# Performance work log

Measured on AMD Instinct MI355X. Metric: run time of the kernel, lower is better.

The kernel has to match this reference:

```python
import jax, jax.numpy as jnp
import numpy as np

B, S, D = 8, 1024, 1024      # batch, seq_len, inp_dim
H, HD = 8, 64                # head_num, head_dim
HID = H * HD                 # hidden_dim = 512
P = 2 * D                    # p_factor * inp_dim = 2048
K = 4                        # causal conv kernel size
EPS = 1e-6
CAP = 15.0                   # soft cap for i/f gates


def _layernorm(x, g, b):
    mu = jnp.mean(x, -1, keepdims=True)
    var = jnp.var(x, -1, keepdims=True)
    return (x - mu) * jax.lax.rsqrt(var + EPS) * g + b


def _soft_cap(v):
    return CAP * jnp.tanh(v / CAP)


def _causal_conv_feat(x, w, b):
    # Conv1d(1,1,K) applied over the FEATURE axis of each timestep (as in the
    # torch code: x_t.unsqueeze(1) -> (bs,1,P)), causal left pad of K-1.
    L = x.shape[-1]
    xp = jnp.pad(x, ((0, 0), (0, 0), (K - 1, 0)))
    out = b
    for m in range(K):
        out = out + w[m] * xp[..., m:m + L]
    return out


def _forward(x, ln_g, ln_b, mh_g, mh_b, W_up_l, b_up_l, W_up_r, b_up_r,
             W_down, b_down, conv_w, conv_b, W_skip, b_skip, W_i, b_i,
             W_f, b_f, W_o, b_o, W_q, b_q, W_k, b_k, W_v, b_v):
    Bs, Sl, _ = x.shape
    xn = _layernorm(x, ln_g, ln_b)
    x_t = xn @ W_up_l.T + b_up_l                      # (B,S,P)
    r_t = xn @ W_up_r.T + b_up_r                      # (B,S,HID)
    x_c = jax.nn.silu(_causal_conv_feat(x_t, conv_w, conv_b))
    x_skip = x_c @ W_skip.T + b_skip                  # (B,S,HID)
    q = (x_c @ W_q.T + b_q).reshape(Bs, Sl, H, HD)
    k = (x_c @ W_k.T + b_k).reshape(Bs, Sl, H, HD) / float(np.sqrt(HD))
    v = (x_t @ W_v.T + b_v).reshape(Bs, Sl, H, HD)
    i_pre = _soft_cap(x_c @ W_i.T + b_i)              # (B,S,H)
    f_pre = _soft_cap(x_c @ W_f.T + b_f)              # (B,S,H)
    o = jax.nn.sigmoid(x_t @ W_o.T + b_o)             # (B,S,HID)

    def step(carry, inp):
        c, n, m = carry
        qt, kt, vt, it, ft = inp
        m_t = jnp.maximum(ft + m, it)
        ie = jnp.exp(it - m_t)
        fe = jnp.exp(ft - m_t + m)
        c = fe[:, :, None, None] * c + ie[:, :, None, None] * jnp.einsum('bhd,bhe->bhde', vt, kt)
        n = fe[:, :, None] * n + ie[:, :, None] * kt
        num = jnp.einsum('bhde,bhe->bhd', c, qt)
        den = jnp.maximum(jnp.sum(n * qt, -1, keepdims=True), 1.0)
        return (c, n, m_t), num / den

    c0 = jnp.zeros((Bs, H, HD, HD), x.dtype)
    n0 = jnp.ones((Bs, H, HD), x.dtype)
    m0 = jnp.zeros((Bs, H), x.dtype)
    seq = tuple(jnp.moveaxis(a, 1, 0) for a in (q, k, v, i_pre, f_pre))
    _, hs = jax.lax.scan(step, (c0, n0, m0), seq)     # hs: (S,B,H,HD)
    h = o * jnp.moveaxis(hs, 0, 1).reshape(Bs, Sl, HID)
    hn = _layernorm(h.reshape(Bs, Sl, H, HD), mh_g, mh_b).reshape(Bs, Sl, HID)
    out = (hn + x_skip) * jax.nn.silu(r_t)
    return out @ W_down.T + b_down + x


def setup_inputs() -> dict:
    key = jax.random.key(0)
    ks = jax.random.split(key, 16)

    def w(kk, shape):
        return jax.random.normal(kk, shape, jnp.float32) / np.sqrt(shape[-1]).astype(np.float32)

    return {
        'x': jax.random.normal(ks[0], (B, S, D), jnp.float32),
        'ln_g': jnp.ones((D,), jnp.float32), 'ln_b': jnp.zeros((D,), jnp.float32),
        'mh_g': jnp.ones((H, HD), jnp.float32), 'mh_b': jnp.zeros((H, HD), jnp.float32),
        'W_up_l': w(ks[1], (P, D)), 'b_up_l': jnp.zeros((P,), jnp.float32),
        'W_up_r': w(ks[2], (HID, D)), 'b_up_r': jnp.zeros((HID,), jnp.float32),
        'W_down': w(ks[3], (D, HID)), 'b_down': jnp.zeros((D,), jnp.float32),
        'conv_w': jax.random.normal(ks[4], (K,), jnp.float32) * 0.3,
        'conv_b': jnp.zeros((), jnp.float32),
        'W_skip': w(ks[5], (HID, P)), 'b_skip': jnp.zeros((HID,), jnp.float32),
        'W_i': w(ks[6], (H, P)), 'b_i': jnp.zeros((H,), jnp.float32),
        'W_f': w(ks[7], (H, P)), 'b_f': jnp.zeros((H,), jnp.float32),
        'W_o': w(ks[8], (HID, P)), 'b_o': jnp.zeros((HID,), jnp.float32),
        'W_q': w(ks[9], (HID, P)), 'b_q': jnp.zeros((HID,), jnp.float32),
        'W_k': w(ks[10], (HID, P)), 'b_k': jnp.zeros((HID,), jnp.float32),
        'W_v': w(ks[11], (HID, P)), 'b_v': jnp.zeros((HID,), jnp.float32),
    }


def reference(x, ln_g, ln_b, mh_g, mh_b, W_up_l, b_up_l, W_up_r, b_up_r,
              W_down, b_down, conv_w, conv_b, W_skip, b_skip, W_i, b_i,
              W_f, b_f, W_o, b_o, W_q, b_q, W_k, b_k, W_v, b_v):
    return _forward(x, ln_g, ln_b, mh_g, mh_b, W_up_l, b_up_l, W_up_r, b_up_r,
                    W_down, b_down, conv_w, conv_b, W_skip, b_skip, W_i, b_i,
                    W_f, b_f, W_o, b_o, W_q, b_q, W_k, b_k, W_v, b_v)
```

## Files before the change

kernel.cpp:

```cpp
#include <hip/hip_runtime.h>
#include <hip/hip_bf16.h>
#include <math.h>

#define Bq 8
#define Sq 1024
#define Dq 1024
#define Hq 8
#define HDq 64
#define HIDq 512
#define Pq 2048
#define EPSq 1e-6f
#define CAPq 15.0f
#define NCq 16
#define CLq 64
#define ARENA_SH 4096
#define BUF_SH   (4 * ARENA_SH)
#define GEMM_SMEM_BYTES (2 * BUF_SH * 2)

typedef __attribute__((ext_vector_type(8))) short short8;
typedef __attribute__((ext_vector_type(4))) float f32x4v;
typedef __hip_bfloat16 bf16;

__device__ inline void split2(float v, bf16& h, bf16& l) {
  h = __float2bfloat16(v);
  l = __float2bfloat16(v - __bfloat162float(h));
}

__device__ inline float bfs2f(short s) {
  bf16 t = *(const bf16*)&s;
  return __bfloat162float(t);
}

__global__ __launch_bounds__(256) void cvtw_all(
    const float* __restrict__ s0, const float* __restrict__ s1,
    const float* __restrict__ s2, const float* __restrict__ s3,
    const float* __restrict__ s4, const float* __restrict__ s5,
    const float* __restrict__ s6, const float* __restrict__ s7,
    bf16* __restrict__ hi, bf16* __restrict__ lo)
{
  int u = blockIdx.x * 256 + threadIdx.x;
  const float* src; int segBase;
  if      (u <  524288) { src = s0; segBase = 0;       }
  else if (u <  655360) { src = s1; segBase = 524288;  }
  else if (u <  917504) { src = s2; segBase = 655360;  }
  else if (u < 1179648) { src = s3; segBase = 917504;  }
  else if (u < 1441792) { src = s4; segBase = 1179648; }
  else if (u < 1703936) { src = s5; segBase = 1441792; }
  else if (u < 1966080) { src = s6; segBase = 1703936; }
  else                  { src = s7; segBase = 1966080; }
  float4 v = ((const float4*)src)[u - segBase];
  size_t o = (size_t)u * 4;
  bf16 h, l;
  split2(v.x, h, l); hi[o+0] = h; lo[o+0] = l;
  split2(v.y, h, l); hi[o+1] = h; lo[o+1] = l;
  split2(v.z, h, l); hi[o+2] = h; lo[o+2] = l;
  split2(v.w, h, l); hi[o+3] = h; lo[o+3] = l;
}

__global__ __launch_bounds__(256) void ln_kernel(const float* __restrict__ x,
    const float* __restrict__ g, const float* __restrict__ b,
    bf16* __restrict__ yh, bf16* __restrict__ yl)
{
  int row = blockIdx.x;
  int tid = threadIdx.x;
  const float* xr = x + (size_t)row * Dq;
  float v[4]; float s = 0.f, s2 = 0.f;
  #pragma unroll
  for (int i = 0; i < 4; i++) { v[i] = xr[tid + 256*i]; s += v[i]; s2 += v[i]*v[i]; }
  #pragma unroll
  for (int mm = 32; mm > 0; mm >>= 1) { s += __shfl_xor(s, mm, 64); s2 += __shfl_xor(s2, mm, 64); }
  __shared__ float rs[4], rs2[4];
  int lane = tid & 63, wave = tid >> 6;
  if (lane == 0) { rs[wave] = s; rs2[wave] = s2; }
  __syncthreads();
  s  = rs[0] + rs[1] + rs[2] + rs[3];
  s2 = rs2[0] + rs2[1] + rs2[2] + rs2[3];
  float mu  = s * (1.f / Dq);
  float var = s2 * (1.f / Dq) - mu * mu;
  float r = rsqrtf(var + EPSq);
  #pragma unroll
  for (int i = 0; i < 4; i++) {
    int c = tid + 256*i;
    float y = (v[i] - mu) * r * g[c] + b[c];
    bf16 h, l; split2(y, h, l);
    yh[(size_t)row * Dq + c] = h;
    yl[(size_t)row * Dq + c] = l;
  }
}

__device__ __forceinline__ void stage_arena(short* ldsArena, const short* g,
                                            int Kd, int k0, int lane)
{
  int rsub = lane >> 2;
  int cs = (lane & 3) ^ ((lane >> 3) & 3);
  const short* gp = g + (size_t)rsub * Kd + k0 + cs * 8;
  short* lp = ldsArena;
  #pragma unroll
  for (int j = 0; j < 8; j++) {
    __builtin_amdgcn_global_load_lds(
        (const __attribute__((address_space(1))) void*)gp,
        (__attribute__((address_space(3))) void*)lp, 16, 0, 0);
    gp += (size_t)16 * Kd;
    lp += 512;
  }
}

__global__ __launch_bounds__(256) void gemm_x3(
    const bf16* __restrict__ Ahi, const bf16* __restrict__ Alo,
    const bf16* __restrict__ Whi, const bf16* __restrict__ Wlo,
    int Kd, int start1, int start2, const float* __restrict__ resid,
    const float* bias0, float* f0, bf16* h0, bf16* l0, int w0, float sc0, int a0,
    const float* bias1, float* f1, bf16* h1, bf16* l1, int w1, float sc1, int a1,
    const float* bias2, float* f2, bf16* h2, bf16* l2, int w2, float sc2, int a2)
{
  extern __shared__ short smem[];
  int tid = threadIdx.x;
  int lane = tid & 63, wave = tid >> 6;
  int wr = wave >> 1, wc = wave & 1;

  int gx = gridDim.x;
  int flat = blockIdx.y * gx + blockIdx.x;
  int nb = gx * gridDim.y;
  int chunk = nb >> 3;
  int nid = (flat & 7) * chunk + (flat >> 3);
  int col = nid % gx, row = nid / gx;
  int rowBase = row * 128;
  int colBase = col * 128;

  const short* Ahg = (const short*)Ahi + (size_t)rowBase * Kd;
  const short* Alg = (const short*)Alo + (size_t)rowBase * Kd;
  const short* Bhg = (const short*)Whi + (size_t)colBase * Kd;
  const short* Blg = (const short*)Wlo + (size_t)colBase * Kd;

  const short* src = (wave == 0) ? Ahg : (wave == 1) ? Alg
                   : (wave == 2) ? Bhg : Blg;
  short* arena0 = smem + wave * ARENA_SH;
  short* arena1 = smem + BUF_SH + wave * ARENA_SH;

  f32x4v acc[4][4];
  #pragma unroll
  for (int i = 0; i < 4; i++)
    #pragma unroll
    for (int j = 0; j < 4; j++) acc[i][j] = (f32x4v){0.f, 0.f, 0.f, 0.f};

  int fr = lane & 15;
  int cch = lane >> 4;
  int slotOff = ((cch ^ ((fr >> 1) & 3)) << 3);
  int nk = Kd >> 5;

  stage_arena(arena0, src, Kd, 0, lane);
  asm volatile("s_waitcnt vmcnt(0)" ::: "memory");
  __builtin_amdgcn_s_barrier();

  for (int t = 0; t < nk; ++t) {
    const short* Cb = smem + (t & 1) * BUF_SH;
    short* nxt = (t & 1) ? arena0 : arena1;
    if (t + 1 < nk) stage_arena(nxt, src, Kd, (t + 1) * 32, lane);

    short8 afh[4], afl[4], bfh[4], bfl[4];
    #pragma unroll
    for (int mi = 0; mi < 4; mi++) {
      int Ra = (wr * 64 + mi * 16 + fr) * 32;
      afh[mi] = *(const short8*)&Cb[0 * ARENA_SH + Ra + slotOff];
      afl[mi] = *(const short8*)&Cb[1 * ARENA_SH + Ra + slotOff];
    }
    #pragma unroll
    for (int ni = 0; ni < 4; ni++) {
      int Rb = (wc * 64 + ni * 16 + fr) * 32;
      bfh[ni] = *(const short8*)&Cb[2 * ARENA_SH + Rb + slotOff];
      bfl[ni] = *(const short8*)&Cb[3 * ARENA_SH + Rb + slotOff];
    }
    #pragma unroll
    for (int mi = 0; mi < 4; mi++)
      #pragma unroll
      for (int ni = 0; ni < 4; ni++)
        acc[mi][ni] = __builtin_amdgcn_mfma_f32_16x16x32_bf16(afh[mi], bfh[ni], acc[mi][ni], 0, 0, 0);
    #pragma unroll
    for (int mi = 0; mi < 4; mi++)
      #pragma unroll
      for (int ni = 0; ni < 4; ni++)
        acc[mi][ni] = __builtin_amdgcn_mfma_f32_16x16x32_bf16(afh[mi], bfl[ni], acc[mi][ni], 0, 0, 0);
    #pragma unroll
    for (int mi = 0; mi < 4; mi++)
      #pragma unroll
      for (int ni = 0; ni < 4; ni++)
        acc[mi][ni] = __builtin_amdgcn_mfma_f32_16x16x32_bf16(afl[mi], bfh[ni], acc[mi][ni], 0, 0, 0);

    asm volatile("s_waitcnt vmcnt(0)" ::: "memory");
    __builtin_amdgcn_s_barrier();
  }

  const float* bias; float* fOut; bf16* hOut; bf16* lOut; int segStart, segW; float sscale; int sact;
  if (colBase >= start2)      { bias=bias2; fOut=f2; hOut=h2; lOut=l2; segStart=start2; segW=w2; sscale=sc2; sact=a2; }
  else if (colBase >= start1) { bias=bias1; fOut=f1; hOut=h1; lOut=l1; segStart=start1; segW=w1; sscale=sc1; sact=a1; }
  else                        { bias=bias0; fOut=f0; hOut=h0; lOut=l0; segStart=0;      segW=w0; sscale=sc0; sact=a0; }

  int cr = (lane >> 4) * 4;
  int cc = lane & 15;
  #pragma unroll
  for (int mi = 0; mi < 4; mi++) {
    #pragma unroll
    for (int ni = 0; ni < 4; ni++) {
      int colO  = colBase + wc * 64 + ni * 16 + cc;
      int colL = colO - segStart;
      float bv = bias[colL];
      #pragma unroll
      for (int j = 0; j < 4; j++) {
        int rowO = rowBase + wr * 64 + mi * 16 + cr + j;
        float val = (acc[mi][ni][j] + bv) * sscale;
        if (sact) val = 1.f / (1.f + expf(-val));
        if (resid && segStart == 0) val += resid[(size_t)rowO * segW + colL];
        size_t oidx = (size_t)rowO * segW + colL;
        if (fOut) fOut[oidx] = val;
        if (hOut) {
          bf16 h, l; split2(val, h, l);
          hOut[oidx] = h; lOut[oidx] = l;
        }
      }
    }
  }
}

__global__ __launch_bounds__(256) void conv_kernel(const bf16* __restrict__ xth,
    const bf16* __restrict__ xtl, const float* __restrict__ cw,
    const float* __restrict__ cb, bf16* __restrict__ xch, bf16* __restrict__ xcl,
    int total8)
{
  int u = blockIdx.x * 256 + threadIdx.x;
  if (u >= total8) return;
  size_t idx = (size_t)u * 8;
  int p0 = (int)(idx & (Pq - 1));
  const short* hp = (const short*)xth + idx;
  const short* lp = (const short*)xtl + idx;
  short8 ch = *(const short8*)hp;
  short8 cl = *(const short8*)lp;
  float xv[11];
  #pragma unroll
  for (int j = 0; j < 8; j++) xv[3 + j] = bfs2f(ch[j]) + bfs2f(cl[j]);
  if (p0 > 0) {
    short8 ph = *(const short8*)(hp - 8);
    short8 pl = *(const short8*)(lp - 8);
    xv[0] = bfs2f(ph[5]) + bfs2f(pl[5]);
    xv[1] = bfs2f(ph[6]) + bfs2f(pl[6]);
    xv[2] = bfs2f(ph[7]) + bfs2f(pl[7]);
  } else {
    xv[0] = xv[1] = xv[2] = 0.f;
  }
  float w0 = cw[0], w1 = cw[1], w2 = cw[2], w3 = cw[3], bb = cb[0];
  short8 oh, ol;
  #pragma unroll
  for (int j = 0; j < 8; j++) {
    float acc = bb + w3 * xv[j + 3] + w2 * xv[j + 2] + w1 * xv[j + 1] + w0 * xv[j];
    float y = acc / (1.f + expf(-acc));
    bf16 h, l; split2(y, h, l);
    oh[j] = *(const short*)&h;
    ol[j] = *(const short*)&l;
  }
  *(short8*)((short*)xch + idx) = oh;
  *(short8*)((short*)xcl + idx) = ol;
}

__global__ __launch_bounds__(256) void ifk_kernel(const bf16* __restrict__ xch,
    const bf16* __restrict__ xcl,
    const float* __restrict__ Wi, const float* __restrict__ bi,
    const float* __restrict__ Wf, const float* __restrict__ bf_,
    float* __restrict__ ip, float* __restrict__ fp)
{
  int row = blockIdx.x;
  int lane = threadIdx.x & 63, wave = threadIdx.x >> 6;
  size_t rb = (size_t)row * Pq;
  const short* xh = (const short*)xch + rb;
  const short* xl = (const short*)xcl + rb;
  for (int oi = wave; oi < 16; oi += 4) {
    int hh = oi & 7;
    const float* Wrow = (oi < 8) ? (Wi + (size_t)hh * Pq) : (Wf + (size_t)hh * Pq);
    float s = 0.f;
    for (int j0 = lane * 8; j0 < Pq; j0 += 512) {
      short8 hv = *(const short8*)(xh + j0);
      short8 lv = *(const short8*)(xl + j0);
      float4 wa = *(const float4*)(Wrow + j0);
      float4 wb = *(const float4*)(Wrow + j0 + 4);
      s += (bfs2f(hv[0]) + bfs2f(lv[0])) * wa.x;
      s += (bfs2f(hv[1]) + bfs2f(lv[1])) * wa.y;
      s += (bfs2f(hv[2]) + bfs2f(lv[2])) * wa.z;
      s += (bfs2f(hv[3]) + bfs2f(lv[3])) * wa.w;
      s += (bfs2f(hv[4]) + bfs2f(lv[4])) * wb.x;
      s += (bfs2f(hv[5]) + bfs2f(lv[5])) * wb.y;
      s += (bfs2f(hv[6]) + bfs2f(lv[6])) * wb.z;
      s += (bfs2f(hv[7]) + bfs2f(lv[7])) * wb.w;
    }
    #pragma unroll
    for (int mm = 32; mm > 0; mm >>= 1) s += __shfl_xor(s, mm, 64);
    if (lane == 0) {
      float val = s + ((oi < 8) ? bi[hh] : bf_[hh]);
      val = CAPq * tanhf(val / CAPq);
      if (oi < 8) ip[(size_t)row * Hq + hh] = val;
      else        fp[(size_t)row * Hq + hh] = val;
    }
  }
}

__global__ __launch_bounds__(256) void chunkA_kernel(const float* __restrict__ k,
    const float* __restrict__ v, const float* __restrict__ ip,
    const float* __restrict__ fp, float* __restrict__ bg,
    float* __restrict__ FcMc, float* __restrict__ kvg, float* __restrict__ ksumg)
{
  int blk = blockIdx.x;
  int bh = blk >> 4, c = blk & 15;
  int b = bh >> 3, hh = bh & 7;
  int tid = threadIdx.x, lane = tid & 63, wave = tid >> 6;

  __shared__ float sK[64][64], sV[64][64], sW[64];

  size_t base = (size_t)b * Sq * 512 + (size_t)hh * 64 + (size_t)c * CLq * 512;
  int tr = tid >> 4, c4 = (tid & 15) * 4;
  #pragma unroll
  for (int p = 0; p < 4; p++) {
    int t = p * 16 + tr;
    *(float4*)&sK[t][c4] = *(const float4*)(k + base + (size_t)t * 512 + c4);
    *(float4*)&sV[t][c4] = *(const float4*)(v + base + (size_t)t * 512 + c4);
  }
  if (tid < 64) {
    size_t ifb = ((size_t)b * Sq + c * CLq + tid) * Hq + hh;
    float fv = fp[ifb], iv = ip[ifb];
    float cf = fv;
    #pragma unroll
    for (int off = 1; off < 64; off <<= 1) {
      float t2 = __shfl_up(cf, off, 64);
      if (lane >= off) cf += t2;
    }
    float bs = iv - cf;
    float mx = bs;
    #pragma unroll
    for (int off = 1; off < 64; off <<= 1) {
      float t2 = __shfl_up(mx, off, 64);
      if (lane >= off) mx = fmaxf(mx, t2);
    }
    float Mc = __shfl(mx, 63, 64);
    bg[(size_t)blk * 64 + tid] = bs;
    sW[tid] = expf(bs - Mc);
    if (tid == 63) { FcMc[blk*2] = cf; FcMc[blk*2+1] = Mc; }
  }
  __syncthreads();
  float acc[16];
  #pragma unroll
  for (int j = 0; j < 16; j++) acc[j] = 0.f;
  for (int s = 0; s < 64; s++) {
    float wv = sW[s] * sV[s][lane];
    #pragma unroll
    for (int j = 0; j < 16; j++) acc[j] += wv * sK[s][wave*16+j];
  }
  float* kvp = kvg + (size_t)blk * 4096 + lane * 64 + wave * 16;
  #pragma unroll
  for (int j = 0; j < 16; j++) kvp[j] = acc[j];
  if (tid < 64) {
    float a = 0.f;
    for (int s = 0; s < 64; s++) a += sW[s] * sK[s][tid];
    ksumg[(size_t)blk * 64 + tid] = a;
  }
}

__global__ __launch_bounds__(1024) void chunkB_kernel(const float* __restrict__ kvg,
    const float* __restrict__ ksumg, const float* __restrict__ FcMc,
    float* __restrict__ boundC, float* __restrict__ boundN, float* __restrict__ boundM)
{
  int bh = blockIdx.x;
  int tid = threadIdx.x;
  int r  = tid >> 4;
  int cq = (tid & 15) * 4;
  float4 C4 = {0.f, 0.f, 0.f, 0.f};
  float ne = 1.0f, m = 0.f;
  for (int c = 0; c < NCq; c++) {
    size_t blk = (size_t)bh * NCq + c;
    *(float4*)(boundC + blk * 4096 + r * 64 + cq) = C4;
    if ((tid & 15) == 0) boundN[blk * 64 + r] = ne;
    if (tid == 0)        boundM[blk] = m;
    float Fc = FcMc[blk * 2], Mc = FcMc[blk * 2 + 1];
    float mm = fmaxf(m, Mc);
    float a1 = expf(m - mm), a2 = expf(Mc - mm);
    float4 kv = *(const float4*)(kvg + blk * 4096 + r * 64 + cq);
    C4.x = a1 * C4.x + a2 * kv.x;
    C4.y = a1 * C4.y + a2 * kv.y;
    C4.z = a1 * C4.z + a2 * kv.z;
    C4.w = a1 * C4.w + a2 * kv.w;
    ne = a1 * ne + a2 * ksumg[blk * 64 + r];
    m = Fc + mm;
  }
}

__global__ __launch_bounds__(256) void chunkC_kernel(const float* q,
    const float* __restrict__ k, const float* __restrict__ v,
    const float* __restrict__ bg, const float* __restrict__ boundC,
    const float* __restrict__ boundN, const float* __restrict__ boundM,
    float* hs)
{
  int blk = blockIdx.x;
  int bh = blk >> 4, c = blk & 15;
  int b = bh >> 3, hh = bh & 7;
  int tid = threadIdx.x, lane = tid & 63, wave = tid >> 6;

  __shared__ float sQ[64][65], sKV[64][65], sS[64][65];
  __shared__ float sB[64], sMr[64], sNin[64];

  size_t base = (size_t)b * Sq * 512 + (size_t)hh * 64 + (size_t)c * CLq * 512;
  int tr = tid >> 4, c4 = (tid & 15) * 4;
  #pragma unroll
  for (int p = 0; p < 4; p++) {
    int t = p * 16 + tr;
    float4 qv = *(const float4*)(q + base + (size_t)t * 512 + c4);
    float4 kv = *(const float4*)(k + base + (size_t)t * 512 + c4);
    sQ[t][c4+0] = qv.x; sQ[t][c4+1] = qv.y; sQ[t][c4+2] = qv.z; sQ[t][c4+3] = qv.w;
    sKV[t][c4+0] = kv.x; sKV[t][c4+1] = kv.y; sKV[t][c4+2] = kv.z; sKV[t][c4+3] = kv.w;
  }
  float m_in = boundM[blk];
  if (tid < 64) {
    float bs = bg[(size_t)blk * 64 + tid];
    float mx = bs;
    #pragma unroll
    for (int off = 1; off < 64; off <<= 1) {
      float t2 = __shfl_up(mx, off, 64);
      if (lane >= off) mx = fmaxf(mx, t2);
    }
    sB[tid]   = bs;
    sMr[tid]  = fmaxf(m_in, mx);
    sNin[tid] = boundN[(size_t)blk * 64 + tid];
  }
  __syncthreads();

  {
    int t = lane;
    float acc[16];
    #pragma unroll
    for (int j = 0; j < 16; j++) acc[j] = 0.f;
    for (int d = 0; d < 64; d++) {
      float qv = sQ[t][d];
      #pragma unroll
      for (int j = 0; j < 16; j++) acc[j] += qv * sKV[wave*16+j][d];
    }
    float Mr = sMr[t];
    #pragma unroll
    for (int j = 0; j < 16; j++) {
      int s = wave * 16 + j;
      float w = (s <= t) ? expf(sB[s] - Mr) : 0.f;
      sS[t][s] = w * acc[j];
    }
  }
  __syncthreads();
  #pragma unroll
  for (int p = 0; p < 4; p++) {
    int t = p * 16 + tr;
    float4 vv = *(const float4*)(v + base + (size_t)t * 512 + c4);
    sKV[t][c4+0] = vv.x; sKV[t][c4+1] = vv.y; sKV[t][c4+2] = vv.z; sKV[t][c4+3] = vv.w;
  }
  __syncthreads();

  {
    int t = lane;
    float Mr = sMr[t];
    float bfac = expf(m_in - Mr);
    float den = 0.f;
    for (int d = 0; d < 64; d++) den += sNin[d] * sQ[t][d];
    den *= bfac;
    float num[16];
    #pragma unroll
    for (int j = 0; j < 16; j++) num[j] = 0.f;
    const float* Crow = boundC + (size_t)blk * 4096;
    for (int e = 0; e < 64; e++) {
      float qv = sQ[t][e];
      #pragma unroll
      for (int j = 0; j < 16; j++)
        num[j] += Crow[(size_t)(wave*16+j) * 64 + e] * qv;
    }
    #pragma unroll
    for (int j = 0; j < 16; j++) num[j] *= bfac;
    for (int s = 0; s < 64; s++) {
      float ws = sS[t][s];
      den += ws;
      #pragma unroll
      for (int j = 0; j < 16; j++) num[j] += ws * sKV[s][wave*16+j];
    }
    den = fmaxf(den, 1.0f);
    float o[16];
    #pragma unroll
    for (int j = 0; j < 16; j++) o[j] = num[j] / den;
    float* hp = hs + base + (size_t)t * 512 + wave * 16;
    #pragma unroll
    for (int j4 = 0; j4 < 4; j4++)
      ((float4*)hp)[j4] = ((float4*)o)[j4];
  }
}

__global__ __launch_bounds__(256) void epi_kernel(const float* __restrict__ hsv,
    const float* __restrict__ ov, const float* __restrict__ xs,
    const float* __restrict__ rt, const float* __restrict__ mg,
    const float* __restrict__ mb, bf16* __restrict__ pdh, bf16* __restrict__ pdl)
{
  int tid = threadIdx.x;
  int lane = tid & 63, wave = tid >> 6;
  size_t row = (size_t)blockIdx.x * 4 + wave;
  int hh = (int)(row & 7);
  size_t idx = row * 64 + lane;
  float hv = ov[idx] * hsv[idx];
  float s = hv, s2 = hv * hv;
  #pragma unroll
  for (int mm = 32; mm > 0; mm >>= 1) { s += __shfl_xor(s, mm, 64); s2 += __shfl_xor(s2, mm, 64); }
  float mu  = s * (1.f / 64.f);
  float var = s2 * (1.f / 64.f) - mu * mu;
  float r = rsqrtf(var + EPSq);
  float hn = (hv - mu) * r * mg[hh * 64 + lane] + mb[hh * 64 + lane];
  float rv = rt[idx];
  float y = (hn + xs[idx]) * (rv / (1.f + expf(-rv)));
  bf16 h, l; split2(y, h, l);
  pdh[idx] = h; pdl[idx] = l;
}

extern "C" void kernel_launch(void* const* d_in, const int* in_sizes, int n_in,
                              void* d_out, int out_size, void* d_ws, size_t ws_size,
                              hipStream_t stream)
{
  const float* x      = (const float*)d_in[0];
  const float* ln_g   = (const float*)d_in[1];
  const float* ln_b   = (const float*)d_in[2];
  const float* mh_g   = (const float*)d_in[3];
  const float* mh_b   = (const float*)d_in[4];
  const float* W_up_l = (const float*)d_in[5];
  const float* b_up_l = (const float*)d_in[6];
  const float* W_up_r = (const float*)d_in[7];
  const float* b_up_r = (const float*)d_in[8];
  const float* W_down = (const float*)d_in[9];
  const float* b_down = (const float*)d_in[10];
  const float* conv_w = (const float*)d_in[11];
  const float* conv_b = (const float*)d_in[12];
  const float* W_skip = (const float*)d_in[13];
  const float* b_skip = (const float*)d_in[14];
  const float* W_i    = (const float*)d_in[15];
  const float* b_i    = (const float*)d_in[16];
  const float* W_f    = (const float*)d_in[17];
  const float* b_f    = (const float*)d_in[18];
  const float* W_o    = (const float*)d_in[19];
  const float* b_o    = (const float*)d_in[20];
  const float* W_q    = (const float*)d_in[21];
  const float* b_q    = (const float*)d_in[22];
  const float* W_k    = (const float*)d_in[23];
  const float* b_k    = (const float*)d_in[24];
  const float* W_v    = (const float*)d_in[25];
  const float* b_v    = (const float*)d_in[26];
  float* out = (float*)d_out;

  const size_t MB = 1u << 20;
  if (ws_size < 193 * MB) return;

  char* base = (char*)d_ws;
  bf16* whi = (bf16*)base;
  bf16* wlo = (bf16*)(base + 16*MB);
  bf16* xnh = (bf16*)(base + 32*MB);
  bf16* xnl = (bf16*)(base + 48*MB);
  bf16* xth = (bf16*)(base + 64*MB);
  bf16* xtl = (bf16*)(base + 96*MB);
  bf16* xch = (bf16*)(base + 128*MB);
  bf16* xcl = (bf16*)(base + 160*MB);
  float* vb  = (float*)(base + 32*MB);
  float* ob  = (float*)(base + 48*MB);
  float* xs  = (float*)(base + 64*MB);
  float* qb  = (float*)(base + 80*MB);
  float* kb  = (float*)(base + 96*MB);
  bf16*  pdh = (bf16*)(base + 112*MB);
  bf16*  pdl = (bf16*)(base + 120*MB);
  float* kvg    = (float*)(base + 128*MB);
  float* boundC = (float*)(base + 144*MB);
  float* bg     = (float*)(base + 160*MB);
  float* ksumg  = (float*)(base + 160*MB + 256*1024);
  float* boundN = (float*)(base + 160*MB + 512*1024);
  float* FcMc   = (float*)(base + 160*MB + 768*1024);
  float* boundM = (float*)(base + 160*MB + 776*1024);
  float* ip  = (float*)(base + 192*MB);
  float* fpb = (float*)(base + 192*MB + 256*1024);
  float* rt  = out;
  float* hsb = qb;

  const int Mrows = Bq * Sq;
  const int BIG = 1 << 30;

  cvtw_all<<<dim3(8192), dim3(256), 0, stream>>>(
      W_up_l, W_up_r, W_v, W_o, W_skip, W_q, W_k, W_down, whi, wlo);

  ln_kernel<<<dim3(Mrows), dim3(256), 0, stream>>>(x, ln_g, ln_b, xnh, xnl);

  gemm_x3<<<dim3(20, 64), dim3(256), GEMM_SMEM_BYTES, stream>>>(
      xnh, xnl, whi, wlo, 1024, 2048, BIG, nullptr,
      b_up_l, nullptr, xth, xtl, 2048, 1.f, 0,
      b_up_r, rt, nullptr, nullptr, 512, 1.f, 0,
      nullptr, nullptr, nullptr, nullptr, 1, 1.f, 0);

  gemm_x3<<<dim3(8, 64), dim3(256), GEMM_SMEM_BYTES, stream>>>(
      xth, xtl, whi + 2621440, wlo + 2621440, 2048, 512, BIG, nullptr,
      b_v, vb, nullptr, nullptr, 512, 1.f, 0,
      b_o, ob, nullptr, nullptr, 512, 1.f, 1,
      nullptr, nullptr, nullptr, nullptr, 1, 1.f, 0);

  int convTotal8 = Mrows * Pq / 8;
  conv_kernel<<<dim3(convTotal8 / 256), dim3(256), 0, stream>>>(
      xth, xtl, conv_w, conv_b, xch, xcl, convTotal8);

  gemm_x3<<<dim3(12, 64), dim3(256), GEMM_SMEM_BYTES, stream>>>(
      xch, xcl, whi + 4718592, wlo + 4718592, 2048, 512, 1024, nullptr,
      b_skip, xs, nullptr, nullptr, 512, 1.f, 0,
      b_q, qb, nullptr, nullptr, 512, 1.f, 0,
      b_k, kb, nullptr, nullptr, 512, 0.125f, 0);

  ifk_kernel<<<dim3(Mrows), dim3(256), 0, stream>>>(
      xch, xcl, W_i, b_i, W_f, b_f, ip, fpb);

  chunkA_kernel<<<dim3(Bq * Hq * NCq), dim3(256), 0, stream>>>(
      kb, vb, ip, fpb, bg, FcMc, kvg, ksumg);
  chunkB_kernel<<<dim3(Bq * Hq), dim3(1024), 0, stream>>>(
      kvg, ksumg, FcMc, boundC, boundN, boundM);
  chunkC_kernel<<<dim3(Bq * Hq * NCq), dim3(256), 0, stream>>>(
      qb, kb, vb, bg, boundC, boundN, boundM, hsb);

  epi_kernel<<<dim3(Mrows * Hq / 4), dim3(256), 0, stream>>>(
      hsb, ob, xs, rt, mh_g, mh_b, pdh, pdl);

  gemm_x3<<<dim3(8, 64), dim3(256), GEMM_SMEM_BYTES, stream>>>(
      pdh, pdl, whi + 7864320, wlo + 7864320, 512, BIG, BIG, x,
      b_down, out, nullptr, nullptr, 1024, 1.f, 0,
      nullptr, nullptr, nullptr, nullptr, 1, 1.f, 0,
      nullptr, nullptr, nullptr, nullptr, 1, 1.f, 0);
}
```

Baseline: 843.6 us.

## Fuse causal conv with i/f gate projection and chunk output with epilogue

The feature-axis conv+SiLU kernel now also computes the i/f gate projections from registers, using the W_i/W_f weights staged in shared memory. This removes the separate ifk pass that re-read the whole conv output. The chunk output kernel also applies the o-gate, per-head layernorm, skip add and SiLU(r) gating directly, so the hidden state is no longer written and re-read by a separate epilogue kernel. In exchange, the conv kernel uses about 130KB of dynamic shared memory with 512 threads, which limits occupancy, and it adds two block barriers per row pair.

```diff
diff --git a/kernel.cpp b/kernel.cpp
--- a/kernel.cpp
+++ b/kernel.cpp
@@ -16,6 +16,8 @@
 #define ARENA_SH 4096
 #define BUF_SH   (4 * ARENA_SH)
 #define GEMM_SMEM_BYTES (2 * BUF_SH * 2)
+#define WCH 130
+#define CONVIFK_SMEM_BYTES (256 * WCH * 4)
 
 typedef __attribute__((ext_vector_type(8))) short short8;
 typedef __attribute__((ext_vector_type(4))) float f32x4v;
@@ -221,82 +223,100 @@
   }
 }
 
-__global__ __launch_bounds__(256) void conv_kernel(const bf16* __restrict__ xth,
-    const bf16* __restrict__ xtl, const float* __restrict__ cw,
-    const float* __restrict__ cb, bf16* __restrict__ xch, bf16* __restrict__ xcl,
-    int total8)
-{
-  int u = blockIdx.x * 256 + threadIdx.x;
-  if (u >= total8) return;
-  size_t idx = (size_t)u * 8;
-  int p0 = (int)(idx & (Pq - 1));
-  const short* hp = (const short*)xth + idx;
-  const short* lp = (const short*)xtl + idx;
-  short8 ch = *(const short8*)hp;
-  short8 cl = *(const short8*)lp;
-  float xv[11];
-  #pragma unroll
-  for (int j = 0; j < 8; j++) xv[3 + j] = bfs2f(ch[j]) + bfs2f(cl[j]);
-  if (p0 > 0) {
-    short8 ph = *(const short8*)(hp - 8);
-    short8 pl = *(const short8*)(lp - 8);
-    xv[0] = bfs2f(ph[5]) + bfs2f(pl[5]);
-    xv[1] = bfs2f(ph[6]) + bfs2f(pl[6]);
-    xv[2] = bfs2f(ph[7]) + bfs2f(pl[7]);
-  } else {
-    xv[0] = xv[1] = xv[2] = 0.f;
-  }
-  float w0 = cw[0], w1 = cw[1], w2 = cw[2], w3 = cw[3], bb = cb[0];
-  short8 oh, ol;
-  #pragma unroll
-  for (int j = 0; j < 8; j++) {
-    float acc = bb + w3 * xv[j + 3] + w2 * xv[j + 2] + w1 * xv[j + 1] + w0 * xv[j];
-    float y = acc / (1.f + expf(-acc));
-    bf16 h, l; split2(y, h, l);
-    oh[j] = *(const short*)&h;
-    ol[j] = *(const short*)&l;
-  }
-  *(short8*)((short*)xch + idx) = oh;
-  *(short8*)((short*)xcl + idx) = ol;
-}
-
-__global__ __launch_bounds__(256) void ifk_kernel(const bf16* __restrict__ xch,
-    const bf16* __restrict__ xcl,
+__global__ __launch_bounds__(512) void convifk_kernel(
+    const bf16* __restrict__ xth, const bf16* __restrict__ xtl,
+    const float* __restrict__ cw, const float* __restrict__ cb,
     const float* __restrict__ Wi, const float* __restrict__ bi,
     const float* __restrict__ Wf, const float* __restrict__ bf_,
+    bf16* __restrict__ xch, bf16* __restrict__ xcl,
     float* __restrict__ ip, float* __restrict__ fp)
 {
-  int row = blockIdx.x;
-  int lane = threadIdx.x & 63, wave = threadIdx.x >> 6;
-  size_t rb = (size_t)row * Pq;
-  const short* xh = (const short*)xch + rb;
-  const short* xl = (const short*)xcl + rb;
-  for (int oi = wave; oi < 16; oi += 4) {
-    int hh = oi & 7;
-    const float* Wrow = (oi < 8) ? (Wi + (size_t)hh * Pq) : (Wf + (size_t)hh * Pq);
-    float s = 0.f;
-    for (int j0 = lane * 8; j0 < Pq; j0 += 512) {
-      short8 hv = *(const short8*)(xh + j0);
-      short8 lv = *(const short8*)(xl + j0);
-      float4 wa = *(const float4*)(Wrow + j0);
-      float4 wb = *(const float4*)(Wrow + j0 + 4);
-      s += (bfs2f(hv[0]) + bfs2f(lv[0])) * wa.x;
-      s += (bfs2f(hv[1]) + bfs2f(lv[1])) * wa.y;
-      s += (bfs2f(hv[2]) + bfs2f(lv[2])) * wa.z;
-      s += (bfs2f(hv[3]) + bfs2f(lv[3])) * wa.w;
-      s += (bfs2f(hv[4]) + bfs2f(lv[4])) * wb.x;
-      s += (bfs2f(hv[5]) + bfs2f(lv[5])) * wb.y;
-      s += (bfs2f(hv[6]) + bfs2f(lv[6])) * wb.z;
-      s += (bfs2f(hv[7]) + bfs2f(lv[7])) * wb.w;
-    }
-    #pragma unroll
-    for (int mm = 32; mm > 0; mm >>= 1) s += __shfl_xor(s, mm, 64);
+  extern __shared__ float sW[];
+  __shared__ float sRed[8][16];
+  int tid = threadIdx.x;
+  int pr = tid >> 8;
+  int u  = tid & 255;
+  int wv = tid >> 6, lane = tid & 63;
+
+  #pragma unroll
+  for (int h8 = 0; h8 < 8; h8++) {
+    int h = pr * 8 + h8;
+    const float* wsrc = (h < 8) ? (Wi + (size_t)h * Pq) : (Wf + (size_t)(h - 8) * Pq);
+    float4 a = *(const float4*)(wsrc + u * 8);
+    float4 b = *(const float4*)(wsrc + u * 8 + 4);
+    float* dst = sW + (size_t)u * WCH + h * 8;
+    *(float4*)dst = a;
+    *(float4*)(dst + 4) = b;
+  }
+  __syncthreads();
+
+  float bb = cb[0], w0 = cw[0], w1 = cw[1], w2 = cw[2], w3 = cw[3];
+  int rowBase = blockIdx.x * 16;
+
+  for (int rp = 0; rp < 8; rp++) {
+    int row = rowBase + rp * 2 + pr;
+    size_t idx = (size_t)row * Pq + (size_t)u * 8;
+    const short* hp = (const short*)xth + idx;
+    const short* lp = (const short*)xtl + idx;
+    short8 chv = *(const short8*)hp;
+    short8 clv = *(const short8*)lp;
+    float xv[11];
+    #pragma unroll
+    for (int j = 0; j < 8; j++) xv[3 + j] = bfs2f(chv[j]) + bfs2f(clv[j]);
+    if (u > 0) {
+      short8 ph = *(const short8*)(hp - 8);
+      short8 pl = *(const short8*)(lp - 8);
+      xv[0] = bfs2f(ph[5]) + bfs2f(pl[5]);
+      xv[1] = bfs2f(ph[6]) + bfs2f(pl[6]);
+      xv[2] = bfs2f(ph[7]) + bfs2f(pl[7]);
+    } else {
+      xv[0] = xv[1] = xv[2] = 0.f;
+    }
+    float xr[8]; short8 oh, ol;
+    #pragma unroll
+    for (int j = 0; j < 8; j++) {
+      float a = bb + w3 * xv[j + 3] + w2 * xv[j + 2] + w1 * xv[j + 1] + w0 * xv[j];
+      float y = a / (1.f + expf(-a));
+      bf16 h, l; split2(y, h, l);
+      oh[j] = *(const short*)&h;
+      ol[j] = *(const short*)&l;
+      xr[j] = __bfloat162float(h) + __bfloat162float(l);
+    }
+    *(short8*)((short*)xch + idx) = oh;
+    *(short8*)((short*)xcl + idx) = ol;
+
+    float pv[16];
+    const float* wch = sW + (size_t)u * WCH;
+    #pragma unroll
+    for (int h = 0; h < 16; h++) {
+      float4 a = *(const float4*)(wch + h * 8);
+      float4 b = *(const float4*)(wch + h * 8 + 4);
+      pv[h] = xr[0]*a.x + xr[1]*a.y + xr[2]*a.z + xr[3]*a.w
+            + xr[4]*b.x + xr[5]*b.y + xr[6]*b.z + xr[7]*b.w;
+    }
+    #pragma unroll
+    for (int h = 0; h < 16; h++) {
+      float v = pv[h];
+      #pragma unroll
+      for (int m = 32; m > 0; m >>= 1) v += __shfl_xor(v, m, 64);
+      pv[h] = v;
+    }
     if (lane == 0) {
-      float val = s + ((oi < 8) ? bi[hh] : bf_[hh]);
+      #pragma unroll
+      for (int h = 0; h < 16; h++) sRed[wv][h] = pv[h];
+    }
+    __syncthreads();
+    if ((wv == 0 || wv == 4) && lane < 16) {
+      int wb = wv;
+      float v = sRed[wb][lane] + sRed[wb+1][lane] + sRed[wb+2][lane] + sRed[wb+3][lane];
+      int hh2 = lane & 7;
+      float val = v + ((lane < 8) ? bi[hh2] : bf_[hh2]);
       val = CAPq * tanhf(val / CAPq);
-      if (oi < 8) ip[(size_t)row * Hq + hh] = val;
-      else        fp[(size_t)row * Hq + hh] = val;
-    }
+      int rw = rowBase + rp * 2 + (wv >> 2);
+      if (lane < 8) ip[(size_t)rw * Hq + hh2] = val;
+      else          fp[(size_t)rw * Hq + hh2] = val;
+    }
+    __syncthreads();
   }
 }
 
@@ -388,11 +408,13 @@
   }
 }
 
-__global__ __launch_bounds__(256) void chunkC_kernel(const float* q,
+__global__ __launch_bounds__(256) void chunkCE_kernel(const float* __restrict__ q,
     const float* __restrict__ k, const float* __restrict__ v,
     const float* __restrict__ bg, const float* __restrict__ boundC,
     const float* __restrict__ boundN, const float* __restrict__ boundM,
-    float* hs)
+    const float* __restrict__ ov, const float* __restrict__ xs,
+    const float* __restrict__ rt, const float* __restrict__ mg,
+    const float* __restrict__ mb, bf16* __restrict__ pdh, bf16* __restrict__ pdl)
 {
   int blk = blockIdx.x;
   int bh = blk >> 4, c = blk & 15;
@@ -401,6 +423,7 @@
 
   __shared__ float sQ[64][65], sKV[64][65], sS[64][65];
   __shared__ float sB[64], sMr[64], sNin[64];
+  __shared__ float sLs[4][64], sLs2[4][64];
 
   size_t base = (size_t)b * Sq * 512 + (size_t)hh * 64 + (size_t)c * CLq * 512;
   int tr = tid >> 4, c4 = (tid & 15) * 4;
@@ -480,38 +503,51 @@
       for (int j = 0; j < 16; j++) num[j] += ws * sKV[s][wave*16+j];
     }
     den = fmaxf(den, 1.0f);
-    float o[16];
-    #pragma unroll
-    for (int j = 0; j < 16; j++) o[j] = num[j] / den;
-    float* hp = hs + base + (size_t)t * 512 + wave * 16;
-    #pragma unroll
-    for (int j4 = 0; j4 < 4; j4++)
-      ((float4*)hp)[j4] = ((float4*)o)[j4];
-  }
-}
-
-__global__ __launch_bounds__(256) void epi_kernel(const float* __restrict__ hsv,
-    const float* __restrict__ ov, const float* __restrict__ xs,
-    const float* __restrict__ rt, const float* __restrict__ mg,
-    const float* __restrict__ mb, bf16* __restrict__ pdh, bf16* __restrict__ pdl)
-{
-  int tid = threadIdx.x;
-  int lane = tid & 63, wave = tid >> 6;
-  size_t row = (size_t)blockIdx.x * 4 + wave;
-  int hh = (int)(row & 7);
-  size_t idx = row * 64 + lane;
-  float hv = ov[idx] * hsv[idx];
-  float s = hv, s2 = hv * hv;
-  #pragma unroll
-  for (int mm = 32; mm > 0; mm >>= 1) { s += __shfl_xor(s, mm, 64); s2 += __shfl_xor(s2, mm, 64); }
-  float mu  = s * (1.f / 64.f);
-  float var = s2 * (1.f / 64.f) - mu * mu;
-  float r = rsqrtf(var + EPSq);
-  float hn = (hv - mu) * r * mg[hh * 64 + lane] + mb[hh * 64 + lane];
-  float rv = rt[idx];
-  float y = (hn + xs[idx]) * (rv / (1.f + expf(-rv)));
-  bf16 h, l; split2(y, h, l);
-  pdh[idx] = h; pdl[idx] = l;
+
+    size_t gidx = base + (size_t)t * 512 + (size_t)wave * 16;
+    float hv[16];
+    float s1 = 0.f, s2 = 0.f;
+    #pragma unroll
+    for (int j4 = 0; j4 < 4; j4++) {
+      float4 og = *(const float4*)(ov + gidx + j4 * 4);
+      float o0 = og.x * (num[j4*4+0] / den);
+      float o1 = og.y * (num[j4*4+1] / den);
+      float o2 = og.z * (num[j4*4+2] / den);
+      float o3 = og.w * (num[j4*4+3] / den);
+      hv[j4*4+0] = o0; hv[j4*4+1] = o1; hv[j4*4+2] = o2; hv[j4*4+3] = o3;
+      s1 += o0 + o1 + o2 + o3;
+      s2 += o0*o0 + o1*o1 + o2*o2 + o3*o3;
+    }
+    sLs[wave][t] = s1; sLs2[wave][t] = s2;
+    __syncthreads();
+    float S  = sLs[0][t] + sLs[1][t] + sLs[2][t] + sLs[3][t];
+    float S2 = sLs2[0][t] + sLs2[1][t] + sLs2[2][t] + sLs2[3][t];
+    float mu  = S * (1.f / 64.f);
+    float var = S2 * (1.f / 64.f) - mu * mu;
+    float rr = rsqrtf(var + EPSq);
+    short8 ohv[2], olv[2];
+    #pragma unroll
+    for (int j4 = 0; j4 < 4; j4++) {
+      float4 xsv = *(const float4*)(xs + gidx + j4 * 4);
+      float4 rtv = *(const float4*)(rt + gidx + j4 * 4);
+      #pragma unroll
+      for (int e = 0; e < 4; e++) {
+        int j = j4 * 4 + e;
+        int d = wave * 16 + j;
+        float hn = (hv[j] - mu) * rr * mg[hh * 64 + d] + mb[hh * 64 + d];
+        float xsj = (e == 0) ? xsv.x : (e == 1) ? xsv.y : (e == 2) ? xsv.z : xsv.w;
+        float rtj = (e == 0) ? rtv.x : (e == 1) ? rtv.y : (e == 2) ? rtv.z : rtv.w;
+        float y = (hn + xsj) * (rtj / (1.f + expf(-rtj)));
+        bf16 h, l; split2(y, h, l);
+        ohv[j >> 3][j & 7] = *(const short*)&h;
+        olv[j >> 3][j & 7] = *(const short*)&l;
+      }
+    }
+    *(short8*)((short*)pdh + gidx) = ohv[0];
+    *(short8*)((short*)pdh + gidx + 8) = ohv[1];
+    *(short8*)((short*)pdl + gidx) = olv[0];
+    *(short8*)((short*)pdl + gidx + 8) = olv[1];
+  }
 }
 
 extern "C" void kernel_launch(void* const* d_in, const int* in_sizes, int n_in,
@@ -550,6 +586,14 @@
   const size_t MB = 1u << 20;
   if (ws_size < 193 * MB) return;
 
+  static bool attrSet = false;
+  if (!attrSet) {
+    (void)hipFuncSetAttribute(reinterpret_cast<const void*>(convifk_kernel),
+                              hipFuncAttributeMaxDynamicSharedMemorySize,
+                              CONVIFK_SMEM_BYTES);
+    attrSet = true;
+  }
+
   char* base = (char*)d_ws;
   bf16* whi = (bf16*)base;
   bf16* wlo = (bf16*)(base + 16*MB);
@@ -576,7 +620,6 @@
   float* ip  = (float*)(base + 192*MB);
   float* fpb = (float*)(base + 192*MB + 256*1024);
   float* rt  = out;
-  float* hsb = qb;
 
   const int Mrows = Bq * Sq;
   const int BIG = 1 << 30;
@@ -598,9 +641,8 @@
       b_o, ob, nullptr, nullptr, 512, 1.f, 1,
       nullptr, nullptr, nullptr, nullptr, 1, 1.f, 0);
 
-  int convTotal8 = Mrows * Pq / 8;
-  conv_kernel<<<dim3(convTotal8 / 256), dim3(256), 0, stream>>>(
-      xth, xtl, conv_w, conv_b, xch, xcl, convTotal8);
+  convifk_kernel<<<dim3(512), dim3(512), CONVIFK_SMEM_BYTES, stream>>>(
+      xth, xtl, conv_w, conv_b, W_i, b_i, W_f, b_f, xch, xcl, ip, fpb);
 
   gemm_x3<<<dim3(12, 64), dim3(256), GEMM_SMEM_BYTES, stream>>>(
       xch, xcl, whi + 4718592, wlo + 4718592, 2048, 512, 1024, nullptr,
@@ -608,18 +650,12 @@
       b_q, qb, nullptr, nullptr, 512, 1.f, 0,
       b_k, kb, nullptr, nullptr, 512, 0.125f, 0);
 
-  ifk_kernel<<<dim3(Mrows), dim3(256), 0, stream>>>(
-      xch, xcl, W_i, b_i, W_f, b_f, ip, fpb);
-
   chunkA_kernel<<<dim3(Bq * Hq * NCq), dim3(256), 0, stream>>>(
       kb, vb, ip, fpb, bg, FcMc, kvg, ksumg);
   chunkB_kernel<<<dim3(Bq * Hq), dim3(1024), 0, stream>>>(
       kvg, ksumg, FcMc, boundC, boundN, boundM);
-  chunkC_kernel<<<dim3(Bq * Hq * NCq), dim3(256), 0, stream>>>(
-      qb, kb, vb, bg, boundC, boundN, boundM, hsb);
-
-  epi_kernel<<<dim3(Mrows * Hq / 4), dim3(256), 0, stream>>>(
-      hsb, ob, xs, rt, mh_g, mh_b, pdh, pdl);
+  chunkCE_kernel<<<dim3(Bq * Hq * NCq), dim3(256), 0, stream>>>(
+      qb, kb, vb, bg, boundC, boundN, boundM, ob, xs, rt, mh_g, mh_b, pdh, pdl);
 
   gemm_x3<<<dim3(8, 64), dim3(256), GEMM_SMEM_BYTES, stream>>>(
       pdh, pdl, whi + 7864320, wlo + 7864320, 512, BIG, BIG, x,
```

Result: slower. 914.9 us (+8.5%).
